# Kernel tuning notes

Hardware: AMD Instinct MI355X
Metric: run time of the kernel (lower is better)

The kernel has to match this reference:

```python
import jax, jax.numpy as jnp
import numpy as np

B, A, N, FIN, H, HEADS, OUT = 32, 64, 121, 12, 128, 4, 256
NL = 2          # transformer encoder layers
LEVELS = 4      # complete ternary tree: N = (3**(LEVELS+1)-1)//2 = 121
EPS = 1e-5


def setup_inputs() -> dict:
    key = jax.random.key(0)
    ks = jax.random.split(key, 10)
    s = 0.02
    # adjacency: complete ternary tree, local node indices, rows [parent, child, branch]
    child = np.arange(1, N)
    parent = (child - 1) // 3
    branch = (child - 1) % 3
    adj = np.stack([parent, child, branch], -1).astype(np.int32)  # (N-1, 3)
    adjacency = jnp.asarray(np.broadcast_to(adj, (B, A, N - 1, 3)).copy())
    perm = jax.random.permutation(ks[0], N)  # torch.randperm(n_nodes) equivalent
    forest = jax.random.normal(ks[1], (B, A, N, FIN), jnp.float32)
    p = lambda k, shape: s * jax.random.normal(k, shape, jnp.float32)
    return dict(
        forest=forest, adjacency=adjacency, perm=perm,
        w_in=p(ks[2], (H, FIN)), b_in=jnp.zeros((H,), jnp.float32),
        qkv_w=p(ks[3], (NL, 3 * H, H)), qkv_b=jnp.zeros((NL, 3 * H), jnp.float32),
        proj_w=p(ks[4], (NL, H, H)), proj_b=jnp.zeros((NL, H), jnp.float32),
        ff1_w=p(ks[5], (NL, H, H)), ff1_b=jnp.zeros((NL, H), jnp.float32),
        ff2_w=p(ks[6], (NL, H, H)), ff2_b=jnp.zeros((NL, H), jnp.float32),
        ln1_g=jnp.ones((NL, H), jnp.float32), ln1_b=jnp.zeros((NL, H), jnp.float32),
        ln2_g=jnp.ones((NL, H), jnp.float32), ln2_b=jnp.zeros((NL, H), jnp.float32),
        w_out=p(ks[7], (OUT, N * H)), b_out=jnp.zeros((OUT,), jnp.float32),
        lnf_g=jnp.ones((OUT,), jnp.float32), lnf_b=jnp.zeros((OUT,), jnp.float32))


def _ln(x, g, b):
    m = x.mean(-1, keepdims=True)
    v = ((x - m) ** 2).mean(-1, keepdims=True)  # biased var, as torch LayerNorm
    return (x - m) * jax.lax.rsqrt(v + EPS) * g + b


def _tree_pe(adjacency):
    """Level-parallel tree positional encoding: pe[child] = pe[parent] with
    bit (depth*3 + branch) set to 1 (depth 0 = first level below root)."""
    parent = adjacency[..., 0]
    branch = adjacency[..., 2]
    pe = jnp.zeros((B, A, N, H), jnp.float32)
    for l in range(1, LEVELS + 1):
        s0 = (3 ** l - 1) // 2          # first node index at level l
        e0 = (3 ** (l + 1) - 1) // 2    # one past last node at level l
        pa = parent[..., s0 - 1:e0 - 1]             # (B, A, n_l) parent local idx
        br = branch[..., s0 - 1:e0 - 1]             # (B, A, n_l) branch 0/1/2
        ppe = jnp.take_along_axis(pe, pa[..., None], axis=2)  # gather parent PE
        bits = jax.nn.one_hot((l - 1) * 3 + br, H, dtype=jnp.float32)
        pe = pe.at[:, :, s0:e0, :].set(ppe + bits)
    return pe


def _mha(x, wqkv, bqkv, wo, bo):
    S = x.shape[0]
    hd = H // HEADS
    qkv = x @ wqkv.T + bqkv
    q, k, v = [t.reshape(S, N, HEADS, hd) for t in jnp.split(qkv, 3, axis=-1)]
    logits = jnp.einsum('bqhd,bkhd->bhqk', q, k) / float(np.sqrt(hd))
    o = jnp.einsum('bhqk,bkhd->bqhd', jax.nn.softmax(logits, -1), v)
    return o.reshape(S, N, H) @ wo.T + bo


def _forward(forest, adjacency, perm, w_in, b_in, qkv_w, qkv_b, proj_w, proj_b,
             ff1_w, ff1_b, ff2_w, ff2_b, ln1_g, ln1_b, ln2_g, ln2_b,
             w_out, b_out, lnf_g, lnf_b):
    x = forest @ w_in.T + b_in + _tree_pe(adjacency)        # (B, A, N, H)
    x = x.reshape(B * A, N, H)[:, perm]                      # token shuffle
    for i in range(NL):  # post-norm encoder layers, relu FFN, dropout=0
        x = _ln(x + _mha(x, qkv_w[i], qkv_b[i], proj_w[i], proj_b[i]), ln1_g[i], ln1_b[i])
        h = jnp.maximum(x @ ff1_w[i].T + ff1_b[i], 0.0)
        x = _ln(x + h @ ff2_w[i].T + ff2_b[i], ln2_g[i], ln2_b[i])
    y = x.reshape(B * A, N * H) @ w_out.T + b_out
    return _ln(y.reshape(B, A, OUT), lnf_g, lnf_b)


def reference(forest, adjacency, perm, w_in, b_in, qkv_w, qkv_b, proj_w, proj_b,
              ff1_w, ff1_b, ff2_w, ff2_b, ln1_g, ln1_b, ln2_g, ln2_b,
              w_out, b_out, lnf_g, lnf_b):
    return _forward(forest, adjacency, perm, w_in, b_in, qkv_w, qkv_b, proj_w, proj_b,
                    ff1_w, ff1_b, ff2_w, ff2_b, ln1_g, ln1_b, ln2_g, ln2_b,
                    w_out, b_out, lnf_g, lnf_b)
```

## Files before the change

kernel.cpp:

```cpp
#include <hip/hip_runtime.h>


typedef unsigned short u16;
typedef __attribute__((ext_vector_type(8))) short bf16x8;
typedef __attribute__((ext_vector_type(4))) float f32x4;
typedef __attribute__((ext_vector_type(4))) unsigned int u32x4;

#define NTOK 121
#define HD 128
#define S_TOT 2048
#define EPSF 1e-5f

__device__ inline u16 f2bf(float f) {
  unsigned u = __float_as_uint(f);
  return (u16)((u + 0x7FFFu + ((u >> 16) & 1u)) >> 16);
}
__device__ inline float bf2f(u16 h) { return __uint_as_float(((unsigned)h) << 16); }

__device__ inline f32x4 mfma16(bf16x8 a, bf16x8 b, f32x4 c) {
  return __builtin_amdgcn_mfma_f32_16x16x32_bf16(a, b, c, 0, 0, 0);
}

__device__ inline unsigned cvt_pk_bf16(float lo, float hi) {
  unsigned r;
  asm("v_cvt_pk_bf16_f32 %0, %1, %2" : "=v"(r) : "v"(lo), "v"(hi));
  return r;
}

__device__ inline f32x4 vmax4(f32x4 a, f32x4 b) {
  f32x4 r;
  r[0] = fmaxf(a[0], b[0]); r[1] = fmaxf(a[1], b[1]);
  r[2] = fmaxf(a[2], b[2]); r[3] = fmaxf(a[3], b[3]);
  return r;
}

__device__ inline void stage16(const void* g, void* l) {
  __builtin_amdgcn_global_load_lds((__attribute__((address_space(1))) void*)g,
                                   (__attribute__((address_space(3))) void*)l,
                                   16, 0, 0);
}

__device__ inline void quad_repack(unsigned pkA, unsigned pkB, int quad,
                                   unsigned& mlo, unsigned& mhi) {
  unsigned y = (quad < 2) ? pkA : pkB;
  unsigned z = (quad < 2) ? pkB : pkA;
  unsigned a16 = (unsigned)__shfl_xor((int)y, 16);
  unsigned a32 = (unsigned)__shfl_xor((int)z, 32);
  unsigned a48 = (unsigned)__shfl_xor((int)z, 48);
  mlo = (quad == 0) ? y   : (quad == 1) ? a48 : (quad == 2) ? a32 : a16;
  mhi = (quad == 0) ? a16 : (quad == 1) ? a32 : (quad == 2) ? a48 : y;
}

__global__ __launch_bounds__(256) void convw_kernel(
    const float* __restrict__ qkvw, const float* __restrict__ projw,
    const float* __restrict__ ff1w, const float* __restrict__ ff2w,
    const float* __restrict__ wout, u16* __restrict__ dst) {
  int i = blockIdx.x * 256 + threadIdx.x;
  float v;
  if (i < 98304) v = qkvw[i];
  else if (i < 131072) v = projw[i - 98304];
  else if (i < 163840) v = ff1w[i - 131072];
  else if (i < 196608) v = ff2w[i - 163840];
  else v = wout[i - 196608];
  dst[i] = f2bf(v);
}

__global__ __launch_bounds__(256) void inproj_kernel(
    const float* __restrict__ forest, const int* __restrict__ adj,
    const int* __restrict__ perm, const float* __restrict__ WIN,
    const float* __restrict__ BIN, u16* __restrict__ X) {
  __shared__ float wf[128 * 12];
  __shared__ float fr[121 * 12];
  __shared__ float pe[121 * 12];
  __shared__ int pm[121];
  int s = blockIdx.x, tid = threadIdx.x;
  const float* fg = forest + (size_t)s * (NTOK * 12);
  const int* ag = adj + (size_t)s * (120 * 3);
  for (int i = tid; i < 128 * 12; i += 256) wf[i] = WIN[i];
  for (int i = tid; i < 121 * 12; i += 256) { fr[i] = fg[i]; pe[i] = 0.f; }
  if (tid < 121) pm[tid] = perm[tid];
  __syncthreads();
  if (tid > 0 && tid < 121) {
    int n = tid;
    int l = (n <= 3) ? 1 : (n <= 12) ? 2 : (n <= 39) ? 3 : 4;
    int cur = n;
    while (cur > 0) {
      int par = ag[(cur - 1) * 3];
      int br = ag[(cur - 1) * 3 + 2];
      pe[n * 12 + (l - 1) * 3 + br] = 1.f;
      cur = par; l--;
    }
  }
  __syncthreads();
  int h = tid & 127;
  for (int base = 0; base < 121; base += 2) {
    int i = base + (tid >> 7);
    if (i < 121) {
      int node = pm[i];
      float v = BIN[h];
#pragma unroll
      for (int k = 0; k < 12; ++k) v += fr[node * 12 + k] * wf[h * 12 + k];
      if (h < 12) v += pe[node * 12 + h];
      X[(size_t)s * (NTOK * HD) + i * HD + h] = f2bf(v);
    }
  }
}

__global__ __launch_bounds__(256, 2) void attn_kernel(
    const u16* __restrict__ X, u16* __restrict__ O,
    const u16* __restrict__ WQKV, const float* __restrict__ QKVB, int layer) {
  __shared__ u16 lds[16384];
  __shared__ u16 xl[15872];
  int tid = threadIdx.x;
  int wave = tid >> 6, lane = tid & 63, l16 = lane & 15, quad = lane >> 4;
  int seq = blockIdx.x >> 1;
  int head = ((blockIdx.x & 1) << 1) | (wave >> 1);
  int half = wave & 1;
  int hs = wave >> 1;
  u16* Kh = lds + hs * 4096;
  u16* Vh = lds + 8192 + hs * 4096;
  const u16* Xs = X + (size_t)seq * (NTOK * HD);
  const f32x4 fz = {0.f, 0.f, 0.f, 0.f};
  const int wbase = layer * 384 + head * 32;
  const u16* WQ = WQKV + (size_t)wbase * HD;
  const u16* WK = WQKV + (size_t)(wbase + 128) * HD;
  const u16* WV = WQKV + (size_t)(wbase + 256) * HD;

  {
    const char* Xb = (const char*)Xs;
#pragma unroll
    for (int j = 0; j < 8; ++j) {
      int i = wave * 8 + j;
      if (i < 31) {
        int n = i * 64 + lane;
        int r = n >> 4, c = n & 15;
        int rc = r > 120 ? 120 : r;
        stage16(Xb + rc * 256 + ((c ^ (r & 7)) << 4), (void*)(xl + i * 512));
      }
    }
  }
  bf16x8 wqf[2][4], wkf[2][4], wvf[2][4];
#pragma unroll
  for (int nt = 0; nt < 2; ++nt)
#pragma unroll
    for (int k = 0; k < 4; ++k) {
      size_t off = (size_t)(nt * 16 + l16) * HD + k * 32 + quad * 8;
      wqf[nt][k] = *(const bf16x8*)(WQ + off);
      wkf[nt][k] = *(const bf16x8*)(WK + off);
      wvf[nt][k] = *(const bf16x8*)(WV + off);
    }
  float kb2[2], vb2[2];
#pragma unroll
  for (int nt = 0; nt < 2; ++nt) {
    kb2[nt] = QKVB[wbase + 128 + nt * 16 + l16];
    vb2[nt] = QKVB[wbase + 256 + nt * 16 + l16];
  }
  const float scl = 0.17677669529663687f * 1.4426950408889634f;
  float qbias[2][4];
#pragma unroll
  for (int nt = 0; nt < 2; ++nt)
#pragma unroll
    for (int r = 0; r < 4; ++r)
      qbias[nt][r] = QKVB[wbase + nt * 16 + quad * 4 + r];
  asm volatile("s_waitcnt vmcnt(0)" ::: "memory");
  __syncthreads();

#pragma unroll 1
  for (int mt = 0; mt < 4; ++mt) {
    int tb = half * 64 + mt * 16;
    int arow = tb + l16; if (arow > 120) arow = 120;
    bf16x8 a[4];
#pragma unroll
    for (int k = 0; k < 4; ++k)
      a[k] = *(const bf16x8*)(xl + arow * 128 + (((k * 4 + quad) ^ (arow & 7)) << 3));
#pragma unroll
    for (int nt = 0; nt < 2; ++nt) {
      f32x4 kacc = fz, vacc = fz;
#pragma unroll
      for (int k = 0; k < 4; ++k) {
        kacc = mfma16(a[k], wkf[nt][k], kacc);
        vacc = mfma16(a[k], wvf[nt][k], vacc);
      }
      int d = nt * 16 + l16;
      int kc = nt * 2 + (l16 >> 3);
#pragma unroll
      for (int r = 0; r < 4; ++r) {
        int t = tb + quad * 4 + r;
        Kh[t * 32 + ((kc ^ (t & 3)) << 3) + (l16 & 7)] = f2bf(kacc[r] + kb2[nt]);
        float vv = (t < NTOK) ? (vacc[r] + vb2[nt]) : 0.f;
        Vh[d * 128 + (((t >> 3) ^ l16) << 3) + (t & 7)] = f2bf(vv);
      }
    }
  }
  __syncthreads();

#pragma unroll 1
  for (int qmt = 0; qmt < 4; ++qmt) {
    int qb = (half * 4 + qmt) * 16;
    int qrow = qb + l16;
    int qrowc = qrow > 120 ? 120 : qrow;
    bf16x8 xb[4];
#pragma unroll
    for (int k = 0; k < 4; ++k)
      xb[k] = *(const bf16x8*)(xl + qrowc * 128 + (((k * 4 + quad) ^ (qrowc & 7)) << 3));
    f32x4 qv[2];
#pragma unroll
    for (int nt = 0; nt < 2; ++nt) {
      f32x4 acc = fz;
#pragma unroll
      for (int k = 0; k < 4; ++k) acc = mfma16(wqf[nt][k], xb[k], acc);
      qv[nt] = acc;
    }
    unsigned qpk[2][2];
#pragma unroll
    for (int nt = 0; nt < 2; ++nt)
#pragma unroll
      for (int r2 = 0; r2 < 2; ++r2)
        qpk[nt][r2] = cvt_pk_bf16((qv[nt][2 * r2] + qbias[nt][2 * r2]) * scl,
                                  (qv[nt][2 * r2 + 1] + qbias[nt][2 * r2 + 1]) * scl);
    u32x4 qu;
#pragma unroll
    for (int r2 = 0; r2 < 2; ++r2) {
      unsigned mlo, mhi;
      quad_repack(qpk[0][r2], qpk[1][r2], quad, mlo, mhi);
      qu[r2] = mlo; qu[2 + r2] = mhi;
    }
    bf16x8 qfrag = __builtin_bit_cast(bf16x8, qu);
    f32x4 lg[8];
#pragma unroll
    for (int nt = 0; nt < 8; ++nt) {
      bf16x8 ka = *(const bf16x8*)(Kh + (nt * 16 + l16) * 32 + ((quad ^ (l16 & 3)) << 3));
      lg[nt] = mfma16(ka, qfrag, fz);
    }
    f32x4 t0 = vmax4(vmax4(lg[0], lg[1]), vmax4(lg[2], lg[3]));
    f32x4 t1 = vmax4(vmax4(lg[4], lg[5]), vmax4(lg[6], lg[7]));
    f32x4 tm = vmax4(t0, t1);
    float mx = fmaxf(fmaxf(tm[0], tm[1]), fmaxf(tm[2], tm[3]));
    mx = fmaxf(mx, __shfl_xor(mx, 16));
    mx = fmaxf(mx, __shfl_xor(mx, 32));
#pragma unroll
    for (int nt = 0; nt < 8; ++nt)
#pragma unroll
      for (int r = 0; r < 4; ++r) {
        float ev = __builtin_amdgcn_exp2f(lg[nt][r] - mx);
        if (nt == 7 && (quad * 4 + r > 8)) ev = 0.f;
        lg[nt][r] = ev;
      }
    f32x4 s4 = (lg[0] + lg[1]) + (lg[2] + lg[3]) + ((lg[4] + lg[5]) + (lg[6] + lg[7]));
    float sum = (s4[0] + s4[1]) + (s4[2] + s4[3]);
    sum += __shfl_xor(sum, 16);
    sum += __shfl_xor(sum, 32);
    float rinv = __builtin_amdgcn_rcpf(sum);
    unsigned pk[8][2];
#pragma unroll
    for (int nt = 0; nt < 8; ++nt)
#pragma unroll
      for (int r2 = 0; r2 < 2; ++r2)
        pk[nt][r2] = cvt_pk_bf16(lg[nt][2 * r2], lg[nt][2 * r2 + 1]);
    f32x4 oacc[2] = {fz, fz};
#pragma unroll
    for (int s = 0; s < 4; ++s) {
      u32x4 pu;
#pragma unroll
      for (int r2 = 0; r2 < 2; ++r2) {
        unsigned mlo, mhi;
        quad_repack(pk[2 * s][r2], pk[2 * s + 1][r2], quad, mlo, mhi);
        pu[r2] = mlo; pu[2 + r2] = mhi;
      }
      bf16x8 pfrag = __builtin_bit_cast(bf16x8, pu);
#pragma unroll
      for (int mt = 0; mt < 2; ++mt) {
        bf16x8 va = *(const bf16x8*)(Vh + (mt * 16 + l16) * 128 + (((s * 4 + quad) ^ l16) << 3));
        oacc[mt] = mfma16(va, pfrag, oacc[mt]);
      }
    }
    if (qrow < NTOK) {
      u16* Op = O + (size_t)seq * (NTOK * HD) + (size_t)qrow * HD + head * 32;
#pragma unroll
      for (int mt = 0; mt < 2; ++mt)
#pragma unroll
        for (int r2 = 0; r2 < 2; ++r2) {
          unsigned w = cvt_pk_bf16(oacc[mt][2 * r2] * rinv, oacc[mt][2 * r2 + 1] * rinv);
          *(unsigned*)(Op + mt * 16 + quad * 4 + 2 * r2) = w;
        }
    }
  }
}

__global__ __launch_bounds__(256) void projln_kernel(
    u16* __restrict__ X, const u16* __restrict__ O,
    const u16* __restrict__ WP, const float* __restrict__ PB,
    const float* __restrict__ G, const float* __restrict__ Bt, int layer) {
  __shared__ u16 as_[32 * 136];
  __shared__ float ct[32 * 132];
  int r0 = blockIdx.x * 32, tid = threadIdx.x;
  int wave = tid >> 6, lane = tid & 63, l16 = lane & 15, quad = lane >> 4;
  const f32x4 fz = {0.f, 0.f, 0.f, 0.f};
  for (int c = tid; c < 32 * 16; c += 256) {
    int row = c >> 4, g = c & 15;
    *(uint4*)(as_ + row * 136 + g * 8) = *(const uint4*)(O + (size_t)(r0 + row) * HD + g * 8);
  }
  __syncthreads();
  f32x4 acc[2][2] = {{fz, fz}, {fz, fz}};
#pragma unroll
  for (int k = 0; k < 4; ++k) {
    bf16x8 a0 = *(const bf16x8*)(as_ + l16 * 136 + k * 32 + quad * 8);
    bf16x8 a1 = *(const bf16x8*)(as_ + (16 + l16) * 136 + k * 32 + quad * 8);
#pragma unroll
    for (int n = 0; n < 2; ++n) {
      int nt = wave * 2 + n;
      bf16x8 bf = *(const bf16x8*)(WP + ((size_t)(layer * 128 + nt * 16 + l16)) * HD + k * 32 + quad * 8);
      acc[0][n] = mfma16(a0, bf, acc[0][n]);
      acc[1][n] = mfma16(a1, bf, acc[1][n]);
    }
  }
  for (int mt = 0; mt < 2; ++mt)
    for (int n = 0; n < 2; ++n) {
      int nt = wave * 2 + n;
#pragma unroll
      for (int r = 0; r < 4; ++r)
        ct[(mt * 16 + quad * 4 + r) * 132 + nt * 16 + l16] = acc[mt][n][r];
    }
  __syncthreads();
  int row = tid >> 3, l8 = tid & 7;
  size_t R = (size_t)(r0 + row);
  float v[16], sum = 0.f, ssq = 0.f;
#pragma unroll
  for (int i = 0; i < 16; ++i) {
    int c = l8 * 16 + i;
    float t = ct[row * 132 + c] + PB[layer * 128 + c] + bf2f(X[R * HD + c]);
    v[i] = t; sum += t; ssq += t * t;
  }
  for (int m = 1; m <= 4; m <<= 1) { sum += __shfl_xor(sum, m, 64); ssq += __shfl_xor(ssq, m, 64); }
  float mean = sum * (1.f / 128.f);
  float var = ssq * (1.f / 128.f) - mean * mean;
  float rstd = rsqrtf(var + EPSF);
#pragma unroll
  for (int i = 0; i < 16; ++i) {
    int c = l8 * 16 + i;
    X[R * HD + c] = f2bf((v[i] - mean) * rstd * G[layer * 128 + c] + Bt[layer * 128 + c]);
  }
}

__global__ __launch_bounds__(256) void ffn_kernel(
    u16* __restrict__ X,
    const u16* __restrict__ W1, const float* __restrict__ B1,
    const u16* __restrict__ W2, const float* __restrict__ B2,
    const float* __restrict__ G, const float* __restrict__ Bt, int layer) {
  __shared__ u16 as_[32 * 136];
  __shared__ u16 hs[32 * 136];
  __shared__ float ct[32 * 132];
  int r0 = blockIdx.x * 32, tid = threadIdx.x;
  int wave = tid >> 6, lane = tid & 63, l16 = lane & 15, quad = lane >> 4;
  const f32x4 fz = {0.f, 0.f, 0.f, 0.f};
  for (int c = tid; c < 32 * 16; c += 256) {
    int row = c >> 4, g = c & 15;
    *(uint4*)(as_ + row * 136 + g * 8) = *(const uint4*)(X + (size_t)(r0 + row) * HD + g * 8);
  }
  __syncthreads();
  f32x4 acc[2][2] = {{fz, fz}, {fz, fz}};
#pragma unroll
  for (int k = 0; k < 4; ++k) {
    bf16x8 a0 = *(const bf16x8*)(as_ + l16 * 136 + k * 32 + quad * 8);
    bf16x8 a1 = *(const bf16x8*)(as_ + (16 + l16) * 136 + k * 32 + quad * 8);
#pragma unroll
    for (int n = 0; n < 2; ++n) {
      int nt = wave * 2 + n;
      bf16x8 bf = *(const bf16x8*)(W1 + ((size_t)(layer * 128 + nt * 16 + l16)) * HD + k * 32 + quad * 8);
      acc[0][n] = mfma16(a0, bf, acc[0][n]);
      acc[1][n] = mfma16(a1, bf, acc[1][n]);
    }
  }
  for (int mt = 0; mt < 2; ++mt)
    for (int n = 0; n < 2; ++n) {
      int nt = wave * 2 + n;
      int col = nt * 16 + l16;
      float b1 = B1[layer * 128 + col];
#pragma unroll
      for (int r = 0; r < 4; ++r)
        hs[(mt * 16 + quad * 4 + r) * 136 + col] = f2bf(fmaxf(acc[mt][n][r] + b1, 0.f));
    }
  __syncthreads();
  f32x4 acc2[2][2] = {{fz, fz}, {fz, fz}};
#pragma unroll
  for (int k = 0; k < 4; ++k) {
    bf16x8 a0 = *(const bf16x8*)(hs + l16 * 136 + k * 32 + quad * 8);
    bf16x8 a1 = *(const bf16x8*)(hs + (16 + l16) * 136 + k * 32 + quad * 8);
#pragma unroll
    for (int n = 0; n < 2; ++n) {
      int nt = wave * 2 + n;
      bf16x8 bf = *(const bf16x8*)(W2 + ((size_t)(layer * 128 + nt * 16 + l16)) * HD + k * 32 + quad * 8);
      acc2[0][n] = mfma16(a0, bf, acc2[0][n]);
      acc2[1][n] = mfma16(a1, bf, acc2[1][n]);
    }
  }
  for (int mt = 0; mt < 2; ++mt)
    for (int n = 0; n < 2; ++n) {
      int nt = wave * 2 + n;
#pragma unroll
      for (int r = 0; r < 4; ++r)
        ct[(mt * 16 + quad * 4 + r) * 132 + nt * 16 + l16] = acc2[mt][n][r];
    }
  __syncthreads();
  int row = tid >> 3, l8 = tid & 7;
  size_t R = (size_t)(r0 + row);
  float v[16], sum = 0.f, ssq = 0.f;
#pragma unroll
  for (int i = 0; i < 16; ++i) {
    int c = l8 * 16 + i;
    float t = ct[row * 132 + c] + B2[layer * 128 + c] + bf2f(as_[row * 136 + c]);
    v[i] = t; sum += t; ssq += t * t;
  }
  for (int m = 1; m <= 4; m <<= 1) { sum += __shfl_xor(sum, m, 64); ssq += __shfl_xor(ssq, m, 64); }
  float mean = sum * (1.f / 128.f);
  float var = ssq * (1.f / 128.f) - mean * mean;
  float rstd = rsqrtf(var + EPSF);
#pragma unroll
  for (int i = 0; i < 16; ++i) {
    int c = l8 * 16 + i;
    X[R * HD + c] = f2bf((v[i] - mean) * rstd * G[layer * 128 + c] + Bt[layer * 128 + c]);
  }
}

__global__ __launch_bounds__(256, 2) void outgemm_kernel(
    const u16* __restrict__ X, const u16* __restrict__ WO, float* __restrict__ PART) {
  __shared__ u16 as_[64 * 136];
  int mtile = blockIdx.x, j = blockIdx.y;
  int tid = threadIdx.x, wave = tid >> 6, lane = tid & 63, l16 = lane & 15, quad = lane >> 4;
  int s0 = mtile * 64;
  int k0 = (j * 484) / 16, k1 = ((j + 1) * 484) / 16;
  const f32x4 fz = {0.f, 0.f, 0.f, 0.f};
  f32x4 acc[4][4];
  for (int a = 0; a < 4; ++a) for (int b = 0; b < 4; ++b) acc[a][b] = fz;
  for (int kb = k0; kb < k1; kb += 4) {
    int nst = (k1 - kb < 4) ? (k1 - kb) : 4;
    __syncthreads();
    int chunks = 64 * 4 * nst;
    for (int c = tid; c < chunks; c += 256) {
      int row = c / (4 * nst), g = c % (4 * nst);
      *(uint4*)(as_ + row * 136 + g * 8) =
          *(const uint4*)(X + (size_t)(s0 + row) * 15488 + kb * 32 + g * 8);
    }
    __syncthreads();
    for (int kk = 0; kk < nst; ++kk) {
      bf16x8 af[4];
#pragma unroll
      for (int mt = 0; mt < 4; ++mt)
        af[mt] = *(const bf16x8*)(as_ + (mt * 16 + l16) * 136 + kk * 32 + quad * 8);
#pragma unroll
      for (int n = 0; n < 4; ++n) {
        int nt = wave * 4 + n;
        bf16x8 bf = *(const bf16x8*)(WO + (size_t)(nt * 16 + l16) * 15488 +
                                     (size_t)(kb + kk) * 32 + quad * 8);
#pragma unroll
        for (int mt = 0; mt < 4; ++mt) acc[mt][n] = mfma16(af[mt], bf, acc[mt][n]);
      }
    }
  }
  for (int mt = 0; mt < 4; ++mt)
    for (int n = 0; n < 4; ++n) {
      int nt = wave * 4 + n;
#pragma unroll
      for (int r = 0; r < 4; ++r) {
        int row = s0 + mt * 16 + quad * 4 + r;
        PART[((size_t)j * 2048 + row) * 256 + nt * 16 + l16] = acc[mt][n][r];
      }
    }
}

__global__ __launch_bounds__(256) void lnf_kernel(
    const float* __restrict__ PART, const float* __restrict__ BO,
    const float* __restrict__ G, const float* __restrict__ Bt, float* __restrict__ OUT) {
  int s = blockIdx.x * 4 + (threadIdx.x >> 6);
  int lane = threadIdx.x & 63;
  float v[4], sum = 0.f, ssq = 0.f;
#pragma unroll
  for (int i = 0; i < 4; ++i) {
    int c = lane + i * 64;
    float t = BO[c];
    for (int jj = 0; jj < 16; ++jj) t += PART[((size_t)jj * 2048 + s) * 256 + c];
    v[i] = t; sum += t; ssq += t * t;
  }
  for (int m = 1; m <= 32; m <<= 1) { sum += __shfl_xor(sum, m, 64); ssq += __shfl_xor(ssq, m, 64); }
  float mean = sum * (1.f / 256.f);
  float var = ssq * (1.f / 256.f) - mean * mean;
  float rstd = rsqrtf(var + EPSF);
#pragma unroll
  for (int i = 0; i < 4; ++i) {
    int c = lane + i * 64;
    OUT[(size_t)s * 256 + c] = (v[i] - mean) * rstd * G[c] + Bt[c];
  }
}

extern "C" void kernel_launch(void* const* d_in, const int* in_sizes, int n_in,
                              void* d_out, int out_size, void* d_ws, size_t ws_size,
                              hipStream_t stream) {
  const float* forest = (const float*)d_in[0];
  const int* adj      = (const int*)d_in[1];
  const int* perm     = (const int*)d_in[2];
  const float* w_in   = (const float*)d_in[3];
  const float* b_in   = (const float*)d_in[4];
  const float* qkv_w  = (const float*)d_in[5];
  const float* qkv_b  = (const float*)d_in[6];
  const float* proj_w = (const float*)d_in[7];
  const float* proj_b = (const float*)d_in[8];
  const float* ff1_w  = (const float*)d_in[9];
  const float* ff1_b  = (const float*)d_in[10];
  const float* ff2_w  = (const float*)d_in[11];
  const float* ff2_b  = (const float*)d_in[12];
  const float* ln1_g  = (const float*)d_in[13];
  const float* ln1_b  = (const float*)d_in[14];
  const float* ln2_g  = (const float*)d_in[15];
  const float* ln2_b  = (const float*)d_in[16];
  const float* w_out  = (const float*)d_in[17];
  const float* b_out  = (const float*)d_in[18];
  const float* lnf_g  = (const float*)d_in[19];
  const float* lnf_b  = (const float*)d_in[20];

  char* ws = (char*)d_ws;
  u16* WB = (u16*)ws;
  u16* X  = (u16*)(ws + 8323072);
  u16* O  = (u16*)(ws + 8323072 + 63438848);
  float* PART = (float*)(ws + 8323072 + 2 * (size_t)63438848);

  u16* WQKV  = WB;
  u16* WPROJ = WB + 98304;
  u16* WFF1  = WB + 131072;
  u16* WFF2  = WB + 163840;
  u16* WOUT  = WB + 196608;

  convw_kernel<<<16256, 256, 0, stream>>>(qkv_w, proj_w, ff1_w, ff2_w, w_out, WB);
  inproj_kernel<<<2048, 256, 0, stream>>>(forest, adj, perm, w_in, b_in, X);
  for (int layer = 0; layer < 2; ++layer) {
    attn_kernel<<<4096, 256, 0, stream>>>(X, O, WQKV, qkv_b, layer);
    projln_kernel<<<7744, 256, 0, stream>>>(X, O, WPROJ, proj_b, ln1_g, ln1_b, layer);
    ffn_kernel<<<7744, 256, 0, stream>>>(X, WFF1, ff1_b, WFF2, ff2_b, ln2_g, ln2_b, layer);
  }
  outgemm_kernel<<<dim3(32, 16), 256, 0, stream>>>(X, WOUT, PART);
  lnf_kernel<<<512, 256, 0, stream>>>(PART, b_out, lnf_g, lnf_b, (float*)d_out);
}
```

Before: 718.5 us.

## Fuse projection+LN1 and FFN+LN2 into one kernel, add MFMA priority hints

Merges the projection+LayerNorm kernel and the FFN+LayerNorm kernel into a single block kernel. The intermediate LN1 output now stays in shared memory instead of being written to X and read back from global memory, and one launch per layer is removed. Bias and gamma vectors are staged in LDS, LN epilogues use vectorized loads and stores, and attention V and output stores are packed into wider writes. s_setprio is wrapped around the MFMA sections in attention. The cost is more LDS per block (extra row and bias buffers), which may reduce occupancy.

```diff
diff --git a/kernel.cpp b/kernel.cpp
--- a/kernel.cpp
+++ b/kernel.cpp
@@ -5,6 +5,7 @@
 typedef __attribute__((ext_vector_type(8))) short bf16x8;
 typedef __attribute__((ext_vector_type(4))) float f32x4;
 typedef __attribute__((ext_vector_type(4))) unsigned int u32x4;
+typedef __attribute__((ext_vector_type(2))) unsigned int u32x2;
 
 #define NTOK 121
 #define HD 128
@@ -16,6 +17,8 @@
   return (u16)((u + 0x7FFFu + ((u >> 16) & 1u)) >> 16);
 }
 __device__ inline float bf2f(u16 h) { return __uint_as_float(((unsigned)h) << 16); }
+__device__ inline float bfu32lo(unsigned u) { return __uint_as_float(u << 16); }
+__device__ inline float bfu32hi(unsigned u) { return __uint_as_float(u & 0xffff0000u); }
 
 __device__ inline f32x4 mfma16(bf16x8 a, bf16x8 b, f32x4 c) {
   return __builtin_amdgcn_mfma_f32_16x16x32_bf16(a, b, c, 0, 0, 0);
@@ -176,20 +179,28 @@
 #pragma unroll
     for (int nt = 0; nt < 2; ++nt) {
       f32x4 kacc = fz, vacc = fz;
+      __builtin_amdgcn_s_setprio(1);
 #pragma unroll
       for (int k = 0; k < 4; ++k) {
         kacc = mfma16(a[k], wkf[nt][k], kacc);
         vacc = mfma16(a[k], wvf[nt][k], vacc);
       }
+      __builtin_amdgcn_s_setprio(0);
       int d = nt * 16 + l16;
       int kc = nt * 2 + (l16 >> 3);
 #pragma unroll
       for (int r = 0; r < 4; ++r) {
         int t = tb + quad * 4 + r;
         Kh[t * 32 + ((kc ^ (t & 3)) << 3) + (l16 & 7)] = f2bf(kacc[r] + kb2[nt]);
-        float vv = (t < NTOK) ? (vacc[r] + vb2[nt]) : 0.f;
-        Vh[d * 128 + (((t >> 3) ^ l16) << 3) + (t & 7)] = f2bf(vv);
-      }
+      }
+      float vv[4];
+#pragma unroll
+      for (int r = 0; r < 4; ++r) {
+        int t = tb + quad * 4 + r;
+        vv[r] = (t < NTOK) ? (vacc[r] + vb2[nt]) : 0.f;
+      }
+      u32x2 vp = { cvt_pk_bf16(vv[0], vv[1]), cvt_pk_bf16(vv[2], vv[3]) };
+      *(u32x2*)(Vh + d * 128 + ((((tb >> 3) + (quad >> 1)) ^ l16) << 3) + (quad & 1) * 4) = vp;
     }
   }
   __syncthreads();
@@ -204,6 +215,7 @@
     for (int k = 0; k < 4; ++k)
       xb[k] = *(const bf16x8*)(xl + qrowc * 128 + (((k * 4 + quad) ^ (qrowc & 7)) << 3));
     f32x4 qv[2];
+    __builtin_amdgcn_s_setprio(1);
 #pragma unroll
     for (int nt = 0; nt < 2; ++nt) {
       f32x4 acc = fz;
@@ -211,6 +223,7 @@
       for (int k = 0; k < 4; ++k) acc = mfma16(wqf[nt][k], xb[k], acc);
       qv[nt] = acc;
     }
+    __builtin_amdgcn_s_setprio(0);
     unsigned qpk[2][2];
 #pragma unroll
     for (int nt = 0; nt < 2; ++nt)
@@ -227,11 +240,13 @@
     }
     bf16x8 qfrag = __builtin_bit_cast(bf16x8, qu);
     f32x4 lg[8];
+    __builtin_amdgcn_s_setprio(1);
 #pragma unroll
     for (int nt = 0; nt < 8; ++nt) {
       bf16x8 ka = *(const bf16x8*)(Kh + (nt * 16 + l16) * 32 + ((quad ^ (l16 & 3)) << 3));
       lg[nt] = mfma16(ka, qfrag, fz);
     }
+    __builtin_amdgcn_s_setprio(0);
     f32x4 t0 = vmax4(vmax4(lg[0], lg[1]), vmax4(lg[2], lg[3]));
     f32x4 t1 = vmax4(vmax4(lg[4], lg[5]), vmax4(lg[6], lg[7]));
     f32x4 tm = vmax4(t0, t1);
@@ -268,157 +283,208 @@
         pu[r2] = mlo; pu[2 + r2] = mhi;
       }
       bf16x8 pfrag = __builtin_bit_cast(bf16x8, pu);
+      __builtin_amdgcn_s_setprio(1);
 #pragma unroll
       for (int mt = 0; mt < 2; ++mt) {
         bf16x8 va = *(const bf16x8*)(Vh + (mt * 16 + l16) * 128 + (((s * 4 + quad) ^ l16) << 3));
         oacc[mt] = mfma16(va, pfrag, oacc[mt]);
       }
+      __builtin_amdgcn_s_setprio(0);
     }
     if (qrow < NTOK) {
       u16* Op = O + (size_t)seq * (NTOK * HD) + (size_t)qrow * HD + head * 32;
 #pragma unroll
-      for (int mt = 0; mt < 2; ++mt)
-#pragma unroll
-        for (int r2 = 0; r2 < 2; ++r2) {
-          unsigned w = cvt_pk_bf16(oacc[mt][2 * r2] * rinv, oacc[mt][2 * r2 + 1] * rinv);
-          *(unsigned*)(Op + mt * 16 + quad * 4 + 2 * r2) = w;
-        }
-    }
-  }
-}
-
-__global__ __launch_bounds__(256) void projln_kernel(
+      for (int mt = 0; mt < 2; ++mt) {
+        u32x2 w = { cvt_pk_bf16(oacc[mt][0] * rinv, oacc[mt][1] * rinv),
+                    cvt_pk_bf16(oacc[mt][2] * rinv, oacc[mt][3] * rinv) };
+        *(u32x2*)(Op + mt * 16 + quad * 4) = w;
+      }
+    }
+  }
+}
+
+__global__ __launch_bounds__(256) void blockln_kernel(
     u16* __restrict__ X, const u16* __restrict__ O,
     const u16* __restrict__ WP, const float* __restrict__ PB,
-    const float* __restrict__ G, const float* __restrict__ Bt, int layer) {
+    const u16* __restrict__ W1, const float* __restrict__ B1,
+    const u16* __restrict__ W2, const float* __restrict__ B2,
+    const float* __restrict__ G1, const float* __restrict__ Bt1,
+    const float* __restrict__ G2, const float* __restrict__ Bt2, int layer) {
   __shared__ u16 as_[32 * 136];
+  __shared__ u16 xr[32 * 136];
+  __shared__ u16 hs[32 * 136];
   __shared__ float ct[32 * 132];
+  __shared__ float bias_[7 * 128];
   int r0 = blockIdx.x * 32, tid = threadIdx.x;
   int wave = tid >> 6, lane = tid & 63, l16 = lane & 15, quad = lane >> 4;
   const f32x4 fz = {0.f, 0.f, 0.f, 0.f};
+  const float* bPB = bias_;
+  const float* bB1 = bias_ + 128;
+  const float* bB2 = bias_ + 256;
+  const float* bG1 = bias_ + 384;
+  const float* bBt1 = bias_ + 512;
+  const float* bG2 = bias_ + 640;
+  const float* bBt2 = bias_ + 768;
+  for (int i = tid; i < 7 * 128; i += 256) {
+    int which = i >> 7, c = i & 127;
+    float v;
+    if (which == 0) v = PB[layer * 128 + c];
+    else if (which == 1) v = B1[layer * 128 + c];
+    else if (which == 2) v = B2[layer * 128 + c];
+    else if (which == 3) v = G1[layer * 128 + c];
+    else if (which == 4) v = Bt1[layer * 128 + c];
+    else if (which == 5) v = G2[layer * 128 + c];
+    else v = Bt2[layer * 128 + c];
+    bias_[i] = v;
+  }
   for (int c = tid; c < 32 * 16; c += 256) {
     int row = c >> 4, g = c & 15;
     *(uint4*)(as_ + row * 136 + g * 8) = *(const uint4*)(O + (size_t)(r0 + row) * HD + g * 8);
-  }
-  __syncthreads();
-  f32x4 acc[2][2] = {{fz, fz}, {fz, fz}};
-#pragma unroll
-  for (int k = 0; k < 4; ++k) {
-    bf16x8 a0 = *(const bf16x8*)(as_ + l16 * 136 + k * 32 + quad * 8);
-    bf16x8 a1 = *(const bf16x8*)(as_ + (16 + l16) * 136 + k * 32 + quad * 8);
-#pragma unroll
-    for (int n = 0; n < 2; ++n) {
-      int nt = wave * 2 + n;
-      bf16x8 bf = *(const bf16x8*)(WP + ((size_t)(layer * 128 + nt * 16 + l16)) * HD + k * 32 + quad * 8);
-      acc[0][n] = mfma16(a0, bf, acc[0][n]);
-      acc[1][n] = mfma16(a1, bf, acc[1][n]);
-    }
-  }
-  for (int mt = 0; mt < 2; ++mt)
-    for (int n = 0; n < 2; ++n) {
-      int nt = wave * 2 + n;
-#pragma unroll
-      for (int r = 0; r < 4; ++r)
-        ct[(mt * 16 + quad * 4 + r) * 132 + nt * 16 + l16] = acc[mt][n][r];
-    }
-  __syncthreads();
-  int row = tid >> 3, l8 = tid & 7;
-  size_t R = (size_t)(r0 + row);
-  float v[16], sum = 0.f, ssq = 0.f;
-#pragma unroll
-  for (int i = 0; i < 16; ++i) {
-    int c = l8 * 16 + i;
-    float t = ct[row * 132 + c] + PB[layer * 128 + c] + bf2f(X[R * HD + c]);
-    v[i] = t; sum += t; ssq += t * t;
-  }
-  for (int m = 1; m <= 4; m <<= 1) { sum += __shfl_xor(sum, m, 64); ssq += __shfl_xor(ssq, m, 64); }
-  float mean = sum * (1.f / 128.f);
-  float var = ssq * (1.f / 128.f) - mean * mean;
-  float rstd = rsqrtf(var + EPSF);
-#pragma unroll
-  for (int i = 0; i < 16; ++i) {
-    int c = l8 * 16 + i;
-    X[R * HD + c] = f2bf((v[i] - mean) * rstd * G[layer * 128 + c] + Bt[layer * 128 + c]);
-  }
-}
-
-__global__ __launch_bounds__(256) void ffn_kernel(
-    u16* __restrict__ X,
-    const u16* __restrict__ W1, const float* __restrict__ B1,
-    const u16* __restrict__ W2, const float* __restrict__ B2,
-    const float* __restrict__ G, const float* __restrict__ Bt, int layer) {
-  __shared__ u16 as_[32 * 136];
-  __shared__ u16 hs[32 * 136];
-  __shared__ float ct[32 * 132];
-  int r0 = blockIdx.x * 32, tid = threadIdx.x;
-  int wave = tid >> 6, lane = tid & 63, l16 = lane & 15, quad = lane >> 4;
-  const f32x4 fz = {0.f, 0.f, 0.f, 0.f};
-  for (int c = tid; c < 32 * 16; c += 256) {
-    int row = c >> 4, g = c & 15;
-    *(uint4*)(as_ + row * 136 + g * 8) = *(const uint4*)(X + (size_t)(r0 + row) * HD + g * 8);
-  }
-  __syncthreads();
-  f32x4 acc[2][2] = {{fz, fz}, {fz, fz}};
-#pragma unroll
-  for (int k = 0; k < 4; ++k) {
-    bf16x8 a0 = *(const bf16x8*)(as_ + l16 * 136 + k * 32 + quad * 8);
-    bf16x8 a1 = *(const bf16x8*)(as_ + (16 + l16) * 136 + k * 32 + quad * 8);
-#pragma unroll
-    for (int n = 0; n < 2; ++n) {
-      int nt = wave * 2 + n;
-      bf16x8 bf = *(const bf16x8*)(W1 + ((size_t)(layer * 128 + nt * 16 + l16)) * HD + k * 32 + quad * 8);
-      acc[0][n] = mfma16(a0, bf, acc[0][n]);
-      acc[1][n] = mfma16(a1, bf, acc[1][n]);
-    }
-  }
-  for (int mt = 0; mt < 2; ++mt)
-    for (int n = 0; n < 2; ++n) {
-      int nt = wave * 2 + n;
-      int col = nt * 16 + l16;
-      float b1 = B1[layer * 128 + col];
-#pragma unroll
-      for (int r = 0; r < 4; ++r)
-        hs[(mt * 16 + quad * 4 + r) * 136 + col] = f2bf(fmaxf(acc[mt][n][r] + b1, 0.f));
-    }
-  __syncthreads();
-  f32x4 acc2[2][2] = {{fz, fz}, {fz, fz}};
-#pragma unroll
-  for (int k = 0; k < 4; ++k) {
-    bf16x8 a0 = *(const bf16x8*)(hs + l16 * 136 + k * 32 + quad * 8);
-    bf16x8 a1 = *(const bf16x8*)(hs + (16 + l16) * 136 + k * 32 + quad * 8);
-#pragma unroll
-    for (int n = 0; n < 2; ++n) {
-      int nt = wave * 2 + n;
-      bf16x8 bf = *(const bf16x8*)(W2 + ((size_t)(layer * 128 + nt * 16 + l16)) * HD + k * 32 + quad * 8);
-      acc2[0][n] = mfma16(a0, bf, acc2[0][n]);
-      acc2[1][n] = mfma16(a1, bf, acc2[1][n]);
-    }
-  }
-  for (int mt = 0; mt < 2; ++mt)
-    for (int n = 0; n < 2; ++n) {
-      int nt = wave * 2 + n;
-#pragma unroll
-      for (int r = 0; r < 4; ++r)
-        ct[(mt * 16 + quad * 4 + r) * 132 + nt * 16 + l16] = acc2[mt][n][r];
-    }
-  __syncthreads();
-  int row = tid >> 3, l8 = tid & 7;
-  size_t R = (size_t)(r0 + row);
-  float v[16], sum = 0.f, ssq = 0.f;
-#pragma unroll
-  for (int i = 0; i < 16; ++i) {
-    int c = l8 * 16 + i;
-    float t = ct[row * 132 + c] + B2[layer * 128 + c] + bf2f(as_[row * 136 + c]);
-    v[i] = t; sum += t; ssq += t * t;
-  }
-  for (int m = 1; m <= 4; m <<= 1) { sum += __shfl_xor(sum, m, 64); ssq += __shfl_xor(ssq, m, 64); }
-  float mean = sum * (1.f / 128.f);
-  float var = ssq * (1.f / 128.f) - mean * mean;
-  float rstd = rsqrtf(var + EPSF);
-#pragma unroll
-  for (int i = 0; i < 16; ++i) {
-    int c = l8 * 16 + i;
-    X[R * HD + c] = f2bf((v[i] - mean) * rstd * G[layer * 128 + c] + Bt[layer * 128 + c]);
+    *(uint4*)(xr + row * 136 + g * 8) = *(const uint4*)(X + (size_t)(r0 + row) * HD + g * 8);
+  }
+  __syncthreads();
+  {
+    f32x4 acc[2][2] = {{fz, fz}, {fz, fz}};
+#pragma unroll
+    for (int k = 0; k < 4; ++k) {
+      bf16x8 a0 = *(const bf16x8*)(as_ + l16 * 136 + k * 32 + quad * 8);
+      bf16x8 a1 = *(const bf16x8*)(as_ + (16 + l16) * 136 + k * 32 + quad * 8);
+#pragma unroll
+      for (int n = 0; n < 2; ++n) {
+        int nt = wave * 2 + n;
+        bf16x8 bf = *(const bf16x8*)(WP + ((size_t)(layer * 128 + nt * 16 + l16)) * HD + k * 32 + quad * 8);
+        acc[0][n] = mfma16(a0, bf, acc[0][n]);
+        acc[1][n] = mfma16(a1, bf, acc[1][n]);
+      }
+    }
+    for (int mt = 0; mt < 2; ++mt)
+      for (int n = 0; n < 2; ++n) {
+        int nt = wave * 2 + n;
+#pragma unroll
+        for (int r = 0; r < 4; ++r)
+          ct[(mt * 16 + quad * 4 + r) * 132 + nt * 16 + l16] = acc[mt][n][r];
+      }
+  }
+  __syncthreads();
+  {
+    int row = tid >> 3, l8 = tid & 7;
+    float cv[16];
+#pragma unroll
+    for (int q = 0; q < 4; ++q) {
+      float4 t4 = *(const float4*)(ct + row * 132 + l8 * 16 + q * 4);
+      cv[q * 4] = t4.x; cv[q * 4 + 1] = t4.y; cv[q * 4 + 2] = t4.z; cv[q * 4 + 3] = t4.w;
+    }
+    uint4 ra = *(const uint4*)(xr + row * 136 + l8 * 16);
+    uint4 rb = *(const uint4*)(xr + row * 136 + l8 * 16 + 8);
+    unsigned rw[8] = {ra.x, ra.y, ra.z, ra.w, rb.x, rb.y, rb.z, rb.w};
+    float v[16], sum = 0.f, ssq = 0.f;
+#pragma unroll
+    for (int j = 0; j < 8; ++j) {
+      int c = l8 * 16 + 2 * j;
+      float t0 = cv[2 * j] + bPB[c] + bfu32lo(rw[j]);
+      float t1 = cv[2 * j + 1] + bPB[c + 1] + bfu32hi(rw[j]);
+      v[2 * j] = t0; v[2 * j + 1] = t1;
+      sum += t0 + t1; ssq += t0 * t0 + t1 * t1;
+    }
+    for (int m = 1; m <= 4; m <<= 1) { sum += __shfl_xor(sum, m, 64); ssq += __shfl_xor(ssq, m, 64); }
+    float mean = sum * (1.f / 128.f);
+    float var = ssq * (1.f / 128.f) - mean * mean;
+    float rstd = rsqrtf(var + EPSF);
+    unsigned w[8];
+#pragma unroll
+    for (int j = 0; j < 8; ++j) {
+      int c = l8 * 16 + 2 * j;
+      float o0 = (v[2 * j] - mean) * rstd * bG1[c] + bBt1[c];
+      float o1 = (v[2 * j + 1] - mean) * rstd * bG1[c + 1] + bBt1[c + 1];
+      w[j] = cvt_pk_bf16(o0, o1);
+    }
+    *(uint4*)(as_ + row * 136 + l8 * 16) = make_uint4(w[0], w[1], w[2], w[3]);
+    *(uint4*)(as_ + row * 136 + l8 * 16 + 8) = make_uint4(w[4], w[5], w[6], w[7]);
+  }
+  __syncthreads();
+  {
+    f32x4 acc[2][2] = {{fz, fz}, {fz, fz}};
+#pragma unroll
+    for (int k = 0; k < 4; ++k) {
+      bf16x8 a0 = *(const bf16x8*)(as_ + l16 * 136 + k * 32 + quad * 8);
+      bf16x8 a1 = *(const bf16x8*)(as_ + (16 + l16) * 136 + k * 32 + quad * 8);
+#pragma unroll
+      for (int n = 0; n < 2; ++n) {
+        int nt = wave * 2 + n;
+        bf16x8 bf = *(const bf16x8*)(W1 + ((size_t)(layer * 128 + nt * 16 + l16)) * HD + k * 32 + quad * 8);
+        acc[0][n] = mfma16(a0, bf, acc[0][n]);
+        acc[1][n] = mfma16(a1, bf, acc[1][n]);
+      }
+    }
+    for (int mt = 0; mt < 2; ++mt)
+      for (int n = 0; n < 2; ++n) {
+        int nt = wave * 2 + n;
+        int col = nt * 16 + l16;
+        float b1 = bB1[col];
+#pragma unroll
+        for (int r = 0; r < 4; ++r)
+          hs[(mt * 16 + quad * 4 + r) * 136 + col] = f2bf(fmaxf(acc[mt][n][r] + b1, 0.f));
+      }
+  }
+  __syncthreads();
+  {
+    f32x4 acc[2][2] = {{fz, fz}, {fz, fz}};
+#pragma unroll
+    for (int k = 0; k < 4; ++k) {
+      bf16x8 a0 = *(const bf16x8*)(hs + l16 * 136 + k * 32 + quad * 8);
+      bf16x8 a1 = *(const bf16x8*)(hs + (16 + l16) * 136 + k * 32 + quad * 8);
+#pragma unroll
+      for (int n = 0; n < 2; ++n) {
+        int nt = wave * 2 + n;
+        bf16x8 bf = *(const bf16x8*)(W2 + ((size_t)(layer * 128 + nt * 16 + l16)) * HD + k * 32 + quad * 8);
+        acc[0][n] = mfma16(a0, bf, acc[0][n]);
+        acc[1][n] = mfma16(a1, bf, acc[1][n]);
+      }
+    }
+    for (int mt = 0; mt < 2; ++mt)
+      for (int n = 0; n < 2; ++n) {
+        int nt = wave * 2 + n;
+#pragma unroll
+        for (int r = 0; r < 4; ++r)
+          ct[(mt * 16 + quad * 4 + r) * 132 + nt * 16 + l16] = acc[mt][n][r];
+      }
+  }
+  __syncthreads();
+  {
+    int row = tid >> 3, l8 = tid & 7;
+    float cv[16];
+#pragma unroll
+    for (int q = 0; q < 4; ++q) {
+      float4 t4 = *(const float4*)(ct + row * 132 + l8 * 16 + q * 4);
+      cv[q * 4] = t4.x; cv[q * 4 + 1] = t4.y; cv[q * 4 + 2] = t4.z; cv[q * 4 + 3] = t4.w;
+    }
+    uint4 ra = *(const uint4*)(as_ + row * 136 + l8 * 16);
+    uint4 rb = *(const uint4*)(as_ + row * 136 + l8 * 16 + 8);
+    unsigned rw[8] = {ra.x, ra.y, ra.z, ra.w, rb.x, rb.y, rb.z, rb.w};
+    float v[16], sum = 0.f, ssq = 0.f;
+#pragma unroll
+    for (int j = 0; j < 8; ++j) {
+      int c = l8 * 16 + 2 * j;
+      float t0 = cv[2 * j] + bB2[c] + bfu32lo(rw[j]);
+      float t1 = cv[2 * j + 1] + bB2[c + 1] + bfu32hi(rw[j]);
+      v[2 * j] = t0; v[2 * j + 1] = t1;
+      sum += t0 + t1; ssq += t0 * t0 + t1 * t1;
+    }
+    for (int m = 1; m <= 4; m <<= 1) { sum += __shfl_xor(sum, m, 64); ssq += __shfl_xor(ssq, m, 64); }
+    float mean = sum * (1.f / 128.f);
+    float var = ssq * (1.f / 128.f) - mean * mean;
+    float rstd = rsqrtf(var + EPSF);
+    unsigned w[8];
+#pragma unroll
+    for (int j = 0; j < 8; ++j) {
+      int c = l8 * 16 + 2 * j;
+      float o0 = (v[2 * j] - mean) * rstd * bG2[c] + bBt2[c];
+      float o1 = (v[2 * j + 1] - mean) * rstd * bG2[c + 1] + bBt2[c + 1];
+      w[j] = cvt_pk_bf16(o0, o1);
+    }
+    size_t R = (size_t)(r0 + row);
+    *(uint4*)(X + R * HD + l8 * 16) = make_uint4(w[0], w[1], w[2], w[3]);
+    *(uint4*)(X + R * HD + l8 * 16 + 8) = make_uint4(w[4], w[5], w[6], w[7]);
   }
 }
 
@@ -533,8 +599,8 @@
   inproj_kernel<<<2048, 256, 0, stream>>>(forest, adj, perm, w_in, b_in, X);
   for (int layer = 0; layer < 2; ++layer) {
     attn_kernel<<<4096, 256, 0, stream>>>(X, O, WQKV, qkv_b, layer);
-    projln_kernel<<<7744, 256, 0, stream>>>(X, O, WPROJ, proj_b, ln1_g, ln1_b, layer);
-    ffn_kernel<<<7744, 256, 0, stream>>>(X, WFF1, ff1_b, WFF2, ff2_b, ln2_g, ln2_b, layer);
+    blockln_kernel<<<7744, 256, 0, stream>>>(X, O, WPROJ, proj_b, WFF1, ff1_b,
+                                             WFF2, ff2_b, ln1_g, ln1_b, ln2_g, ln2_b, layer);
   }
   outgemm_kernel<<<dim3(32, 16), 256, 0, stream>>>(X, WOUT, PART);
   lnf_kernel<<<512, 256, 0, stream>>>(PART, b_out, lnf_g, lnf_b, (float*)d_out);
```

Result: faster. 650.5 us (-9.5%).
